# Kernel optimization log

Hardware: AMD Instinct MI355X
Metric: run time of the kernel (lower is better)

The kernel has to match this reference:

```python
import jax
import jax.numpy as jnp
import numpy as np
from jax import lax

TOKENS = 65536
D = 512
E = 8
H = 2048


def setup_inputs() -> dict:
    key = jax.random.key(0)
    ks = jax.random.split(key, 6)
    inp = {
        "x": jax.random.normal(ks[0], (TOKENS, D), dtype=jnp.float32),
        "router_w": jax.random.normal(ks[1], (D, E), dtype=jnp.float32) * 0.02,
        "router_b": jnp.zeros((E,), dtype=jnp.float32),
        "w1": jax.random.normal(ks[2], (E, D, H), dtype=jnp.float32) * 0.02,
        "b1": jnp.zeros((E, H), dtype=jnp.float32),
        "w2": jax.random.normal(ks[3], (E, H, D), dtype=jnp.float32) * 0.02,
        "b2": jnp.zeros((E, D), dtype=jnp.float32),
        "act_expert_num": 2,
    }
    return inp


def reference(x, router_w, router_b, w1, b1, w2, b2, act_expert_num):
    B = x.shape[0]
    # Router: Linear + Softmax over experts
    probs = jax.nn.softmax(x @ router_w + router_b, axis=-1)  # [B, E]
    rw, sel = lax.top_k(probs, act_expert_num)                # [B, k]
    rw = rw / jnp.sum(rw, axis=-1, keepdims=True)             # renormalize top-k
    # Dense combine weights per expert: comb[b, e] = sum_k rw[b,k] * [sel[b,k]==e]
    comb = jnp.zeros((B, E), dtype=x.dtype).at[
        jnp.arange(B)[:, None], sel
    ].add(rw)                                                 # [B, E]

    def body(acc, params):
        w1e, b1e, w2e, b2e, ce = params
        h = jax.nn.relu(x @ w1e + b1e)        # [B, H]
        y = h @ w2e + b2e                     # [B, D]
        return acc + ce[:, None] * y, None

    out, _ = lax.scan(body, jnp.zeros_like(x), (w1, b1, w2, b2, comb.T))
    return out
```

## Files before the change

kernel.cpp:

```cpp
#include <hip/hip_runtime.h>
#include <hip/hip_bf16.h>

constexpr int B = 65536;
constexpr int D = 512;
constexpr int E = 8;
constexpr int H = 2048;
constexpr int CT_ST = 140;

typedef __bf16 bf16x8 __attribute__((ext_vector_type(8)));
typedef float  f32x4  __attribute__((ext_vector_type(4)));

__device__ __forceinline__ unsigned short f2bf(float f) {
    unsigned u = __float_as_uint(f);
    u += 0x7FFFu + ((u >> 16) & 1u);
    return (unsigned short)(u >> 16);
}

__device__ __forceinline__ void dma16(const void* g, void* lds) {
    auto* gp = reinterpret_cast<const __attribute__((address_space(1))) unsigned*>(
        reinterpret_cast<uintptr_t>(g));
    auto* lp = reinterpret_cast<__attribute__((address_space(3))) unsigned*>(
        reinterpret_cast<uintptr_t>(lds));
    __builtin_amdgcn_global_load_lds(gp, lp, 16, 0, 0);
}

__global__ __launch_bounds__(256) void convert_x(
    const float* __restrict__ x, unsigned short* __restrict__ xb) {
    const size_t i = ((size_t)blockIdx.x * 256 + threadIdx.x) * 8;
    const float4 v0 = *(const float4*)(x + i);
    const float4 v1 = *(const float4*)(x + i + 4);
    uint4 p;
    p.x = (unsigned)f2bf(v0.x) | ((unsigned)f2bf(v0.y) << 16);
    p.y = (unsigned)f2bf(v0.z) | ((unsigned)f2bf(v0.w) << 16);
    p.z = (unsigned)f2bf(v1.x) | ((unsigned)f2bf(v1.y) << 16);
    p.w = (unsigned)f2bf(v1.z) | ((unsigned)f2bf(v1.w) << 16);
    *(uint4*)(xb + i) = p;
}

__global__ __launch_bounds__(128) void router2(
    const float* __restrict__ x, const float* __restrict__ rw,
    const float* __restrict__ rb, unsigned* __restrict__ cnt,
    unsigned* __restrict__ tok_list, float* __restrict__ w_list) {
    __shared__ unsigned lcnt[E];
    __shared__ unsigned gbase[E];
    const int tid = threadIdx.x;
    if (tid < E) lcnt[tid] = 0u;
    __syncthreads();

    const int t = blockIdx.x * 128 + tid;
    const float4* xr = (const float4*)(x + (size_t)t * D);
    float acc[E];
#pragma unroll
    for (int e = 0; e < E; ++e) acc[e] = 0.f;

    for (int i = 0; i < D / 4; ++i) {
        const float4 xv = xr[i];
        const float* wr = rw + (size_t)i * 4 * E;
#pragma unroll
        for (int e = 0; e < E; ++e) {
            acc[e] += xv.x * wr[e] + xv.y * wr[E + e] + xv.z * wr[2 * E + e]
                    + xv.w * wr[3 * E + e];
        }
    }
#pragma unroll
    for (int e = 0; e < E; ++e) acc[e] += rb[e];

    int e0 = 0; float l0 = acc[0];
#pragma unroll
    for (int e = 1; e < E; ++e) if (acc[e] > l0) { l0 = acc[e]; e0 = e; }
    int e1 = -1; float l1 = -3.4e38f;
#pragma unroll
    for (int e = 0; e < E; ++e)
        if (e != e0 && acc[e] > l1) { l1 = acc[e]; e1 = e; }

    const float w0 = 1.f / (1.f + expf(l1 - l0));
    const float w1v = 1.f - w0;

    const unsigned r0 = atomicAdd(&lcnt[e0], 1u);
    const unsigned r1 = atomicAdd(&lcnt[e1], 1u);
    __syncthreads();
    if (tid < E) gbase[tid] = atomicAdd(&cnt[tid], lcnt[tid]);
    __syncthreads();
    const unsigned s0 = gbase[e0] + r0;
    const unsigned s1 = gbase[e1] + r1;
    tok_list[(size_t)e0 * B + s0] = (unsigned)t;  w_list[(size_t)e0 * B + s0] = w0;
    tok_list[(size_t)e1 * B + s1] = (unsigned)t;  w_list[(size_t)e1 * B + s1] = w1v;
}

__global__ __launch_bounds__(128) void pad_counts(
    const unsigned* __restrict__ cnt, unsigned* __restrict__ cntp,
    unsigned* __restrict__ tok_list, float* __restrict__ w_list, int cap) {
    const int tid = threadIdx.x;
    for (int e = 0; e < E; ++e) {
        const unsigned c = cnt[e];
        unsigned p = (c + 127u) & ~127u;
        if (p > (unsigned)cap) p = (unsigned)cap;
        if (c + tid < p) {
            tok_list[(size_t)e * B + c + tid] = 0u;
            w_list[(size_t)e * B + c + tid] = 0.f;
        }
        if (tid == 0) cntp[e] = p;
    }
}

__global__ __launch_bounds__(256) void transpose_bf16(
    const float* __restrict__ in, unsigned short* __restrict__ outp,
    int R, int C) {
    __shared__ unsigned short T[64][72];
    const int e = blockIdx.z;
    const int c0 = blockIdx.x * 64, r0 = blockIdx.y * 64;
    const float* ine = in + (size_t)e * R * C;
    unsigned short* oute = outp + (size_t)e * R * C;
    const int tid = threadIdx.x;
    const int rl = tid >> 2, cl = (tid & 3) * 16;

    const float* src = ine + (size_t)(r0 + rl) * C + c0 + cl;
    unsigned pk[8];
#pragma unroll
    for (int i = 0; i < 4; ++i) {
        const float4 v = *(const float4*)(src + i * 4);
        pk[2 * i]     = (unsigned)f2bf(v.x) | ((unsigned)f2bf(v.y) << 16);
        pk[2 * i + 1] = (unsigned)f2bf(v.z) | ((unsigned)f2bf(v.w) << 16);
    }
    *(uint4*)(&T[rl][cl])     = make_uint4(pk[0], pk[1], pk[2], pk[3]);
    *(uint4*)(&T[rl][cl + 8]) = make_uint4(pk[4], pk[5], pk[6], pk[7]);
    __syncthreads();

    unsigned po[8];
#pragma unroll
    for (int j = 0; j < 8; ++j) {
        po[j] = (unsigned)T[cl + 2 * j][rl] | ((unsigned)T[cl + 2 * j + 1][rl] << 16);
    }
    unsigned short* dst = oute + (size_t)(c0 + rl) * R + r0 + cl;
    *(uint4*)(dst)     = make_uint4(po[0], po[1], po[2], po[3]);
    *(uint4*)(dst + 8) = make_uint4(po[4], po[5], po[6], po[7]);
}

struct alignas(16) StageBufs {
    unsigned short A[2][128 * 32];
    unsigned short Bm[2][128 * 32];
};
union SmemU {
    StageBufs st;
    unsigned short Ct[64 * CT_ST];
};

__global__ __launch_bounds__(256, 4) void stage_kernel(
    const unsigned short* __restrict__ xb,
    const unsigned short* __restrict__ w1s, const unsigned short* __restrict__ w2s,
    const float* __restrict__ b1, const float* __restrict__ b2,
    const unsigned* __restrict__ cntp,
    const unsigned* __restrict__ tok_list, const float* __restrict__ w_list,
    unsigned short* __restrict__ hb_w, const unsigned short* __restrict__ hb_r,
    float* __restrict__ out, int e_w, int e_r) {
    __shared__ SmemU sm;
    __shared__ int   s_toks[128];
    __shared__ float s_wgts[128];
    const int tid = threadIdx.x, wv = tid >> 6, lane = tid & 63;
    const int ln = lane & 15, q = lane >> 4;
    const int wm = wv & 1, wn = wv >> 1;
    const int r4 = lane >> 2, pc = lane & 3;
    const int m0 = blockIdx.x * 128;
    const int dst0 = (wv * 2 + 0) * 512;
    const int dst1 = (wv * 2 + 1) * 512;

    f32x4 acc[4][4];
#pragma unroll
    for (int i = 0; i < 4; ++i)
#pragma unroll
        for (int j = 0; j < 4; ++j) acc[i][j] = (f32x4){0.f, 0.f, 0.f, 0.f};

    if (blockIdx.y >= 4) {
        if (e_w < 0) return;
        const int e = e_w;
        if ((unsigned)m0 >= cntp[e]) return;
        const int n0 = (blockIdx.y - 4) * 128;
        const size_t base = (size_t)e * B;

        const unsigned ta0 = tok_list[base + m0 + (wv * 2 + 0) * 16 + r4];
        const unsigned ta1 = tok_list[base + m0 + (wv * 2 + 1) * 16 + r4];
        const unsigned short* ap0 = xb + (size_t)ta0 * D + pc * 8;
        const unsigned short* ap1 = xb + (size_t)ta1 * D + pc * 8;
        const unsigned short* w1e = w1s + (size_t)e * H * D;
        const unsigned short* bp0 = w1e + (size_t)(n0 + (wv * 2 + 0) * 16 + r4) * D + pc * 8;
        const unsigned short* bp1 = w1e + (size_t)(n0 + (wv * 2 + 1) * 16 + r4) * D + pc * 8;

        unsigned short* Aw = sm.st.A[0];  unsigned short* Bw = sm.st.Bm[0];
        unsigned short* An = sm.st.A[1];  unsigned short* Bn = sm.st.Bm[1];

        dma16(ap0, Aw + dst0);  dma16(ap1, Aw + dst1);
        dma16(bp0, Bw + dst0);  dma16(bp1, Bw + dst1);
        __syncthreads();

#pragma unroll 2
        for (int t = 0; t < D / 32; ++t) {
            if (t < D / 32 - 1) {
                const int nk = (t + 1) * 32;
                dma16(ap0 + nk, An + dst0);  dma16(ap1 + nk, An + dst1);
                dma16(bp0 + nk, Bn + dst0);  dma16(bp1 + nk, Bn + dst1);
            }
            bf16x8 af[4], bfr[4];
#pragma unroll
            for (int i = 0; i < 4; ++i) {
                af[i]  = *(const bf16x8*)(Aw + (wm * 64 + i * 16 + ln) * 32 + q * 8);
                bfr[i] = *(const bf16x8*)(Bw + (wn * 64 + i * 16 + ln) * 32 + q * 8);
            }
#pragma unroll
            for (int mt = 0; mt < 4; ++mt)
#pragma unroll
                for (int nt = 0; nt < 4; ++nt)
                    acc[mt][nt] = __builtin_amdgcn_mfma_f32_16x16x32_bf16(
                        af[mt], bfr[nt], acc[mt][nt], 0, 0, 0);
            __syncthreads();
            unsigned short* tp;
            tp = Aw; Aw = An; An = tp;
            tp = Bw; Bw = Bn; Bn = tp;
        }

        float b1v[4];
#pragma unroll
        for (int nt = 0; nt < 4; ++nt)
            b1v[nt] = b1[(size_t)e * H + n0 + wn * 64 + nt * 16 + ln];

#pragma unroll
        for (int c = 0; c < 2; ++c) {
            if (wm == c) {
#pragma unroll
                for (int mt = 0; mt < 4; ++mt)
#pragma unroll
                    for (int nt = 0; nt < 4; ++nt)
#pragma unroll
                        for (int r = 0; r < 4; ++r) {
                            const int lr = mt * 16 + q * 4 + r;
                            float v = acc[mt][nt][r] + b1v[nt];
                            v = v > 0.f ? v : 0.f;
                            sm.Ct[lr * CT_ST + wn * 64 + nt * 16 + ln] = f2bf(v);
                        }
            }
            __syncthreads();
            {
                const int lr = tid >> 2, seg = tid & 3;
                const unsigned short* csrc = sm.Ct + lr * CT_ST + seg * 32;
                unsigned short* gdst = hb_w + (size_t)(m0 + c * 64 + lr) * H + n0 + seg * 32;
#pragma unroll
                for (int u = 0; u < 4; ++u)
                    *(uint4*)(gdst + u * 8) = *(const uint4*)(csrc + u * 8);
            }
            __syncthreads();
        }
    } else {
        if (e_r < 0) return;
        const int e = e_r;
        if ((unsigned)m0 >= cntp[e]) return;
        const int n0 = blockIdx.y * 128;
        const size_t base = (size_t)e * B;

        if (tid < 128) {
            s_toks[tid] = (int)tok_list[base + m0 + tid];
            s_wgts[tid] = w_list[base + m0 + tid];
        }
        const unsigned short* ap0 = hb_r + (size_t)(m0 + (wv * 2 + 0) * 16 + r4) * H + pc * 8;
        const unsigned short* ap1 = hb_r + (size_t)(m0 + (wv * 2 + 1) * 16 + r4) * H + pc * 8;
        const unsigned short* w2e = w2s + (size_t)e * D * H;
        const unsigned short* bp0 = w2e + (size_t)(n0 + (wv * 2 + 0) * 16 + r4) * H + pc * 8;
        const unsigned short* bp1 = w2e + (size_t)(n0 + (wv * 2 + 1) * 16 + r4) * H + pc * 8;

        unsigned short* Aw = sm.st.A[0];  unsigned short* Bw = sm.st.Bm[0];
        unsigned short* An = sm.st.A[1];  unsigned short* Bn = sm.st.Bm[1];

        dma16(ap0, Aw + dst0);  dma16(ap1, Aw + dst1);
        dma16(bp0, Bw + dst0);  dma16(bp1, Bw + dst1);
        __syncthreads();

#pragma unroll 2
        for (int t = 0; t < H / 32; ++t) {
            if (t < H / 32 - 1) {
                const int nk = (t + 1) * 32;
                dma16(ap0 + nk, An + dst0);  dma16(ap1 + nk, An + dst1);
                dma16(bp0 + nk, Bn + dst0);  dma16(bp1 + nk, Bn + dst1);
            }
            bf16x8 af[4], bfr[4];
#pragma unroll
            for (int i = 0; i < 4; ++i) {
                af[i]  = *(const bf16x8*)(Aw + (wm * 64 + i * 16 + ln) * 32 + q * 8);
                bfr[i] = *(const bf16x8*)(Bw + (wn * 64 + i * 16 + ln) * 32 + q * 8);
            }
#pragma unroll
            for (int mt = 0; mt < 4; ++mt)
#pragma unroll
                for (int nt = 0; nt < 4; ++nt)
                    acc[mt][nt] = __builtin_amdgcn_mfma_f32_16x16x32_bf16(
                        af[mt], bfr[nt], acc[mt][nt], 0, 0, 0);
            __syncthreads();
            unsigned short* tp;
            tp = Aw; Aw = An; An = tp;
            tp = Bw; Bw = Bn; Bn = tp;
        }

        float b2v[4];
#pragma unroll
        for (int nt = 0; nt < 4; ++nt)
            b2v[nt] = b2[(size_t)e * D + n0 + wn * 64 + nt * 16 + ln];

#pragma unroll
        for (int mt = 0; mt < 4; ++mt) {
#pragma unroll
            for (int r = 0; r < 4; ++r) {
                const int m = wm * 64 + mt * 16 + q * 4 + r;
                const float wgt = s_wgts[m];
                if (wgt != 0.f) {
                    const int tok = s_toks[m];
                    float* orow = out + (size_t)tok * D + n0 + wn * 64 + ln;
#pragma unroll
                    for (int nt = 0; nt < 4; ++nt)
                        orow[nt * 16] += wgt * (acc[mt][nt][r] + b2v[nt]);
                }
            }
        }
    }
}

extern "C" void kernel_launch(void* const* d_in, const int* in_sizes, int n_in,
                              void* d_out, int out_size, void* d_ws, size_t ws_size,
                              hipStream_t stream) {
    const float* x  = (const float*)d_in[0];
    const float* rw = (const float*)d_in[1];
    const float* rb = (const float*)d_in[2];
    const float* w1 = (const float*)d_in[3];
    const float* b1 = (const float*)d_in[4];
    const float* w2 = (const float*)d_in[5];
    const float* b2 = (const float*)d_in[6];
    float* out = (float*)d_out;

    char* ws = (char*)d_ws;
    const size_t off_tok = 1024;
    const size_t off_wl  = off_tok + (size_t)E * B * 4;
    const size_t off_w1s = off_wl  + (size_t)E * B * 4;
    const size_t off_w2s = off_w1s + (size_t)E * D * H * 2;
    const size_t off_xb  = off_w2s + (size_t)E * D * H * 2;
    const size_t off_hb  = off_xb  + (size_t)B * D * 2;

    unsigned* cnt      = (unsigned*)ws;
    unsigned* cntp     = (unsigned*)(ws + 256);
    unsigned* tok_list = (unsigned*)(ws + off_tok);
    float*    w_list   = (float*)(ws + off_wl);
    unsigned short* w1s = (unsigned short*)(ws + off_w1s);
    unsigned short* w2s = (unsigned short*)(ws + off_w2s);
    unsigned short* xb  = (unsigned short*)(ws + off_xb);

    const size_t rem = (ws_size > off_hb) ? (ws_size - off_hb) : 0;
    const size_t hrow = (size_t)H * 2;
    int cap; bool pipelined;
    {
        size_t cp = (rem / 2 / hrow) & ~(size_t)127;
        if (cp > 24576) cp = 24576;
        if (cp >= 20480) { pipelined = true; cap = (int)cp; }
        else {
            pipelined = false;
            size_t cs = (rem / hrow) & ~(size_t)127;
            if (cs > 24576) cs = 24576;
            cap = (int)cs;
        }
    }
    unsigned short* hb0 = (unsigned short*)(ws + off_hb);
    unsigned short* hb1 = pipelined ? hb0 + (size_t)cap * H : hb0;

    hipMemsetAsync(ws, 0, 1024, stream);
    hipMemsetAsync(d_out, 0, (size_t)out_size * sizeof(float), stream);

    convert_x<<<(B * D) / 2048, 256, 0, stream>>>(x, xb);
    transpose_bf16<<<dim3(H / 64, D / 64, E), 256, 0, stream>>>(w1, w1s, D, H);
    transpose_bf16<<<dim3(D / 64, H / 64, E), 256, 0, stream>>>(w2, w2s, H, D);
    router2<<<B / 128, 128, 0, stream>>>(x, rw, rb, cnt, tok_list, w_list);
    pad_counts<<<1, 128, 0, stream>>>(cnt, cntp, tok_list, w_list, cap);

    const dim3 sgrid(cap / 128, 20);
    if (pipelined) {
        for (int s = 0; s <= E; ++s) {
            unsigned short* hw = (s & 1) ? hb1 : hb0;
            unsigned short* hr = (s & 1) ? hb0 : hb1;
            stage_kernel<<<sgrid, 256, 0, stream>>>(
                xb, w1s, w2s, b1, b2, cntp, tok_list, w_list,
                hw, hr, out, (s < E) ? s : -1, (s > 0) ? s - 1 : -1);
        }
    } else {
        for (int e = 0; e < E; ++e) {
            stage_kernel<<<sgrid, 256, 0, stream>>>(
                xb, w1s, w2s, b1, b2, cntp, tok_list, w_list,
                hb0, hb0, out, e, -1);
            stage_kernel<<<sgrid, 256, 0, stream>>>(
                xb, w1s, w2s, b1, b2, cntp, tok_list, w_list,
                hb0, hb0, out, -1, e);
        }
    }
}
```

Measured before the change: 1.266 ms.

## Triple-buffer LDS GEMM pipeline with swizzled layout and single barrier

Moves both expert GEMM stages from double to triple LDS buffering. Each step waits on vmcnt and uses one barrier instead of two, issues loads two K-steps ahead, and raises wave priority around the MFMA block. An XOR swizzle on the 16-byte chunk index is applied on both the DMA source and the LDS read side to cut bank conflicts. The cost is more LDS per block, which may lower occupancy under launch_bounds(256,4). The hand-written vmcnt counts also risk ordering mistakes.

```diff
diff --git a/kernel.cpp b/kernel.cpp
--- a/kernel.cpp
+++ b/kernel.cpp
@@ -137,8 +137,8 @@
 }
 
 struct alignas(16) StageBufs {
-    unsigned short A[2][128 * 32];
-    unsigned short Bm[2][128 * 32];
+    unsigned short A[3][128 * 32];
+    unsigned short Bm[3][128 * 32];
 };
 union SmemU {
     StageBufs st;
@@ -163,6 +163,8 @@
     const int m0 = blockIdx.x * 128;
     const int dst0 = (wv * 2 + 0) * 512;
     const int dst1 = (wv * 2 + 1) * 512;
+    const int qs  = q  ^ ((ln >> 1) & 3);
+    const int pcs = pc ^ ((r4 >> 1) & 3);
 
     f32x4 acc[4][4];
 #pragma unroll
@@ -176,46 +178,53 @@
         if ((unsigned)m0 >= cntp[e]) return;
         const int n0 = (blockIdx.y - 4) * 128;
         const size_t base = (size_t)e * B;
+        constexpr int NT = D / 32;
 
         const unsigned ta0 = tok_list[base + m0 + (wv * 2 + 0) * 16 + r4];
         const unsigned ta1 = tok_list[base + m0 + (wv * 2 + 1) * 16 + r4];
-        const unsigned short* ap0 = xb + (size_t)ta0 * D + pc * 8;
-        const unsigned short* ap1 = xb + (size_t)ta1 * D + pc * 8;
+        const unsigned short* ap0 = xb + (size_t)ta0 * D + pcs * 8;
+        const unsigned short* ap1 = xb + (size_t)ta1 * D + pcs * 8;
         const unsigned short* w1e = w1s + (size_t)e * H * D;
-        const unsigned short* bp0 = w1e + (size_t)(n0 + (wv * 2 + 0) * 16 + r4) * D + pc * 8;
-        const unsigned short* bp1 = w1e + (size_t)(n0 + (wv * 2 + 1) * 16 + r4) * D + pc * 8;
-
-        unsigned short* Aw = sm.st.A[0];  unsigned short* Bw = sm.st.Bm[0];
-        unsigned short* An = sm.st.A[1];  unsigned short* Bn = sm.st.Bm[1];
-
-        dma16(ap0, Aw + dst0);  dma16(ap1, Aw + dst1);
-        dma16(bp0, Bw + dst0);  dma16(bp1, Bw + dst1);
-        __syncthreads();
-
-#pragma unroll 2
-        for (int t = 0; t < D / 32; ++t) {
-            if (t < D / 32 - 1) {
-                const int nk = (t + 1) * 32;
-                dma16(ap0 + nk, An + dst0);  dma16(ap1 + nk, An + dst1);
-                dma16(bp0 + nk, Bn + dst0);  dma16(bp1 + nk, Bn + dst1);
+        const unsigned short* bp0 = w1e + (size_t)(n0 + (wv * 2 + 0) * 16 + r4) * D + pcs * 8;
+        const unsigned short* bp1 = w1e + (size_t)(n0 + (wv * 2 + 1) * 16 + r4) * D + pcs * 8;
+
+        unsigned short *A0 = sm.st.A[0], *A1 = sm.st.A[1], *A2 = sm.st.A[2];
+        unsigned short *B0 = sm.st.Bm[0], *B1 = sm.st.Bm[1], *B2 = sm.st.Bm[2];
+
+        dma16(ap0, A0 + dst0);       dma16(ap1, A0 + dst1);
+        dma16(bp0, B0 + dst0);       dma16(bp1, B0 + dst1);
+        dma16(ap0 + 32, A1 + dst0);  dma16(ap1 + 32, A1 + dst1);
+        dma16(bp0 + 32, B1 + dst0);  dma16(bp1 + 32, B1 + dst1);
+
+        for (int t = 0; t < NT; ++t) {
+            if (t + 1 < NT) { asm volatile("s_waitcnt vmcnt(4)" ::: "memory"); }
+            else            { asm volatile("s_waitcnt vmcnt(0)" ::: "memory"); }
+            __builtin_amdgcn_s_barrier();
+            asm volatile("" ::: "memory");
+            if (t + 2 < NT) {
+                const int nk = (t + 2) * 32;
+                dma16(ap0 + nk, A2 + dst0);  dma16(ap1 + nk, A2 + dst1);
+                dma16(bp0 + nk, B2 + dst0);  dma16(bp1 + nk, B2 + dst1);
             }
             bf16x8 af[4], bfr[4];
 #pragma unroll
             for (int i = 0; i < 4; ++i) {
-                af[i]  = *(const bf16x8*)(Aw + (wm * 64 + i * 16 + ln) * 32 + q * 8);
-                bfr[i] = *(const bf16x8*)(Bw + (wn * 64 + i * 16 + ln) * 32 + q * 8);
-            }
+                af[i]  = *(const bf16x8*)(A0 + (wm * 64 + i * 16 + ln) * 32 + qs * 8);
+                bfr[i] = *(const bf16x8*)(B0 + (wn * 64 + i * 16 + ln) * 32 + qs * 8);
+            }
+            __builtin_amdgcn_s_setprio(1);
 #pragma unroll
             for (int mt = 0; mt < 4; ++mt)
 #pragma unroll
                 for (int nt = 0; nt < 4; ++nt)
                     acc[mt][nt] = __builtin_amdgcn_mfma_f32_16x16x32_bf16(
                         af[mt], bfr[nt], acc[mt][nt], 0, 0, 0);
-            __syncthreads();
+            __builtin_amdgcn_s_setprio(0);
             unsigned short* tp;
-            tp = Aw; Aw = An; An = tp;
-            tp = Bw; Bw = Bn; Bn = tp;
-        }
+            tp = A0; A0 = A1; A1 = A2; A2 = tp;
+            tp = B0; B0 = B1; B1 = B2; B2 = tp;
+        }
+        __syncthreads();
 
         float b1v[4];
 #pragma unroll
@@ -254,48 +263,55 @@
         if ((unsigned)m0 >= cntp[e]) return;
         const int n0 = blockIdx.y * 128;
         const size_t base = (size_t)e * B;
+        constexpr int NT = H / 32;
 
         if (tid < 128) {
             s_toks[tid] = (int)tok_list[base + m0 + tid];
             s_wgts[tid] = w_list[base + m0 + tid];
         }
-        const unsigned short* ap0 = hb_r + (size_t)(m0 + (wv * 2 + 0) * 16 + r4) * H + pc * 8;
-        const unsigned short* ap1 = hb_r + (size_t)(m0 + (wv * 2 + 1) * 16 + r4) * H + pc * 8;
+        const unsigned short* ap0 = hb_r + (size_t)(m0 + (wv * 2 + 0) * 16 + r4) * H + pcs * 8;
+        const unsigned short* ap1 = hb_r + (size_t)(m0 + (wv * 2 + 1) * 16 + r4) * H + pcs * 8;
         const unsigned short* w2e = w2s + (size_t)e * D * H;
-        const unsigned short* bp0 = w2e + (size_t)(n0 + (wv * 2 + 0) * 16 + r4) * H + pc * 8;
-        const unsigned short* bp1 = w2e + (size_t)(n0 + (wv * 2 + 1) * 16 + r4) * H + pc * 8;
-
-        unsigned short* Aw = sm.st.A[0];  unsigned short* Bw = sm.st.Bm[0];
-        unsigned short* An = sm.st.A[1];  unsigned short* Bn = sm.st.Bm[1];
-
-        dma16(ap0, Aw + dst0);  dma16(ap1, Aw + dst1);
-        dma16(bp0, Bw + dst0);  dma16(bp1, Bw + dst1);
-        __syncthreads();
-
-#pragma unroll 2
-        for (int t = 0; t < H / 32; ++t) {
-            if (t < H / 32 - 1) {
-                const int nk = (t + 1) * 32;
-                dma16(ap0 + nk, An + dst0);  dma16(ap1 + nk, An + dst1);
-                dma16(bp0 + nk, Bn + dst0);  dma16(bp1 + nk, Bn + dst1);
+        const unsigned short* bp0 = w2e + (size_t)(n0 + (wv * 2 + 0) * 16 + r4) * H + pcs * 8;
+        const unsigned short* bp1 = w2e + (size_t)(n0 + (wv * 2 + 1) * 16 + r4) * H + pcs * 8;
+
+        unsigned short *A0 = sm.st.A[0], *A1 = sm.st.A[1], *A2 = sm.st.A[2];
+        unsigned short *B0 = sm.st.Bm[0], *B1 = sm.st.Bm[1], *B2 = sm.st.Bm[2];
+
+        dma16(ap0, A0 + dst0);       dma16(ap1, A0 + dst1);
+        dma16(bp0, B0 + dst0);       dma16(bp1, B0 + dst1);
+        dma16(ap0 + 32, A1 + dst0);  dma16(ap1 + 32, A1 + dst1);
+        dma16(bp0 + 32, B1 + dst0);  dma16(bp1 + 32, B1 + dst1);
+
+        for (int t = 0; t < NT; ++t) {
+            if (t + 1 < NT) { asm volatile("s_waitcnt vmcnt(4)" ::: "memory"); }
+            else            { asm volatile("s_waitcnt vmcnt(0)" ::: "memory"); }
+            __builtin_amdgcn_s_barrier();
+            asm volatile("" ::: "memory");
+            if (t + 2 < NT) {
+                const int nk = (t + 2) * 32;
+                dma16(ap0 + nk, A2 + dst0);  dma16(ap1 + nk, A2 + dst1);
+                dma16(bp0 + nk, B2 + dst0);  dma16(bp1 + nk, B2 + dst1);
             }
             bf16x8 af[4], bfr[4];
 #pragma unroll
             for (int i = 0; i < 4; ++i) {
-                af[i]  = *(const bf16x8*)(Aw + (wm * 64 + i * 16 + ln) * 32 + q * 8);
-                bfr[i] = *(const bf16x8*)(Bw + (wn * 64 + i * 16 + ln) * 32 + q * 8);
-            }
+                af[i]  = *(const bf16x8*)(A0 + (wm * 64 + i * 16 + ln) * 32 + qs * 8);
+                bfr[i] = *(const bf16x8*)(B0 + (wn * 64 + i * 16 + ln) * 32 + qs * 8);
+            }
+            __builtin_amdgcn_s_setprio(1);
 #pragma unroll
             for (int mt = 0; mt < 4; ++mt)
 #pragma unroll
                 for (int nt = 0; nt < 4; ++nt)
                     acc[mt][nt] = __builtin_amdgcn_mfma_f32_16x16x32_bf16(
                         af[mt], bfr[nt], acc[mt][nt], 0, 0, 0);
-            __syncthreads();
+            __builtin_amdgcn_s_setprio(0);
             unsigned short* tp;
-            tp = Aw; Aw = An; An = tp;
-            tp = Bw; Bw = Bn; Bn = tp;
-        }
+            tp = A0; A0 = A1; A1 = A2; A2 = tp;
+            tp = B0; B0 = B1; B1 = B2; B2 = tp;
+        }
+        __syncthreads();
 
         float b2v[4];
 #pragma unroll
```

Result: slower. 1.316 ms (+4.0%).
